# Optimization experiments

Measured on AMD Instinct MI355X. Metric: run time of the kernel, lower is better.

Reference implementation:

```python
import jax, jax.numpy as jnp
import numpy as np
from jax import lax

N_POINTS = 4_194_304
HIDDEN = 16
N_HIDDEN_LAYERS = 8   # num_layers=9 -> 1 input layer + 8 bias-free hidden layers


def setup_inputs() -> dict:
    key = jax.random.key(0)
    k_x, k_win, k_bin, k_wh, k_wout = jax.random.split(key, 5)
    x = jax.random.uniform(k_x, (N_POINTS, 2), dtype=jnp.float32)
    # PyTorch Linear default init: U(-1/sqrt(fan_in), 1/sqrt(fan_in))
    s_in = 1.0 / np.sqrt(2.0)
    s_h = 1.0 / np.sqrt(HIDDEN)
    W_in = jax.random.uniform(k_win, (HIDDEN, 2), jnp.float32, -s_in, s_in)
    b_in = jax.random.uniform(k_bin, (HIDDEN,), jnp.float32, -s_in, s_in)
    W_hidden = jax.random.uniform(k_wh, (N_HIDDEN_LAYERS, HIDDEN, HIDDEN), jnp.float32, -s_h, s_h)
    W_out = jax.random.uniform(k_wout, (3, HIDDEN), jnp.float32, -s_h, s_h)
    return {"x": x, "W_in": W_in, "b_in": b_in, "W_hidden": W_hidden, "W_out": W_out}


def reference(x, W_in, b_in, W_hidden, W_out):
    # [N,2] -> [N,16], biased input layer + tanh
    h = jnp.tanh(x @ W_in.T + b_in)
    # 8 bias-free 16x16 layers, each followed by tanh
    def step(h, W):
        return jnp.tanh(h @ W.T), None
    h, _ = lax.scan(step, h, W_hidden)
    # output layer 16 -> 3, sigmoid to map to [0,1] RGB
    return jax.nn.sigmoid(h @ W_out.T)
```

## Files before the change

kernel.cpp:

```cpp
#include <hip/hip_runtime.h>


typedef float  f32x4 __attribute__((ext_vector_type(4)));
typedef __fp16 f16x4 __attribute__((ext_vector_type(4)));
typedef __fp16 f16x2 __attribute__((ext_vector_type(2)));

#define K2   2.8853900817779268f
#define KOUT (-1.4426950408889634f)

__device__ __forceinline__ float tanh_from_y(float y) {
    float e = __builtin_amdgcn_exp2f(y);
    float r = __builtin_amdgcn_rcpf(e + 1.0f);
    return __builtin_fmaf(-2.0f, r, 1.0f);
}

__device__ __forceinline__ f16x4 pack4(float a, float b, float c, float d) {
    f16x2 lo = __builtin_amdgcn_cvt_pkrtz(a, b);
    f16x2 hi = __builtin_amdgcn_cvt_pkrtz(c, d);
    return __builtin_shufflevector(lo, hi, 0, 1, 2, 3);
}

__global__ __launch_bounds__(256, 4)
void artnet_kernel(const float2* __restrict__ x,
                   const float2* __restrict__ Win,
                   const float*  __restrict__ bin,
                   const float4* __restrict__ Wh,
                   const float4* __restrict__ Wout,
                   float* __restrict__ out,
                   int nPairs, int nWaves)
{
    const int tid  = blockIdx.x * 256 + threadIdx.x;
    const int gw   = tid >> 6;
    const int lane = threadIdx.x & 63;
    const int row  = lane & 15;
    const int quad = lane >> 4;

    f16x4 aw[8];
#pragma unroll
    for (int l = 0; l < 8; ++l) {
        float4 w = Wh[l * 64 + row * 4 + quad];
        aw[l] = pack4(w.x * K2, w.y * K2, w.z * K2, w.w * K2);
    }

    float wi0[4], wi1[4], bb[4];
#pragma unroll
    for (int j = 0; j < 4; ++j) {
        float2 wr = Win[quad * 4 + j];
        wi0[j] = wr.x * K2;
        wi1[j] = wr.y * K2;
        bb[j]  = bin[quad * 4 + j] * K2;
    }

    float wo0[4], wo1[4], wo2[4];
    {
        float4 w0 = Wout[0 * 4 + quad];
        float4 w1 = Wout[1 * 4 + quad];
        float4 w2 = Wout[2 * 4 + quad];
        wo0[0] = w0.x * KOUT; wo0[1] = w0.y * KOUT; wo0[2] = w0.z * KOUT; wo0[3] = w0.w * KOUT;
        wo1[0] = w1.x * KOUT; wo1[1] = w1.y * KOUT; wo1[2] = w1.z * KOUT; wo1[3] = w1.w * KOUT;
        wo2[0] = w2.x * KOUT; wo2[1] = w2.y * KOUT; wo2[2] = w2.z * KOUT; wo2[3] = w2.w * KOUT;
    }

    const f32x4 zero4 = {0.0f, 0.0f, 0.0f, 0.0f};

    for (int pi = gw; pi < nPairs; pi += nWaves) {
        const int t0 = pi * 2;
        f16x4 bf[2];
        float tl[2][4];

#pragma unroll
        for (int s = 0; s < 2; ++s) {
            float2 xv = x[(t0 + s) * 16 + row];
            float h0 = tanh_from_y(__builtin_fmaf(xv.x, wi0[0], __builtin_fmaf(xv.y, wi1[0], bb[0])));
            float h1 = tanh_from_y(__builtin_fmaf(xv.x, wi0[1], __builtin_fmaf(xv.y, wi1[1], bb[1])));
            float h2 = tanh_from_y(__builtin_fmaf(xv.x, wi0[2], __builtin_fmaf(xv.y, wi1[2], bb[2])));
            float h3 = tanh_from_y(__builtin_fmaf(xv.x, wi0[3], __builtin_fmaf(xv.y, wi1[3], bb[3])));
            bf[s] = pack4(h0, h1, h2, h3);
        }

#pragma unroll
        for (int l = 0; l < 8; ++l) {
#pragma unroll
            for (int s = 0; s < 2; ++s) {
                f32x4 acc = __builtin_amdgcn_mfma_f32_16x16x16f16(aw[l], bf[s], zero4, 0, 0, 0);
                float u0 = tanh_from_y(acc[0]);
                float u1 = tanh_from_y(acc[1]);
                float u2 = tanh_from_y(acc[2]);
                float u3 = tanh_from_y(acc[3]);
                bf[s] = pack4(u0, u1, u2, u3);
                if (l == 7) { tl[s][0] = u0; tl[s][1] = u1; tl[s][2] = u2; tl[s][3] = u3; }
            }
        }

#pragma unroll
        for (int s = 0; s < 2; ++s) {
            float p0 = 0.0f, p1 = 0.0f, p2 = 0.0f;
#pragma unroll
            for (int j = 0; j < 4; ++j) {
                p0 = __builtin_fmaf(tl[s][j], wo0[j], p0);
                p1 = __builtin_fmaf(tl[s][j], wo1[j], p1);
                p2 = __builtin_fmaf(tl[s][j], wo2[j], p2);
            }
            p0 += __shfl_xor(p0, 16, 64); p0 += __shfl_xor(p0, 32, 64);
            p1 += __shfl_xor(p1, 16, 64); p1 += __shfl_xor(p1, 32, 64);
            p2 += __shfl_xor(p2, 16, 64); p2 += __shfl_xor(p2, 32, 64);
            float y  = (quad == 0) ? p0 : ((quad == 1) ? p1 : p2);
            float e  = __builtin_amdgcn_exp2f(y);
            float sg = __builtin_amdgcn_rcpf(e + 1.0f);
            if (quad < 3) {
                out[((t0 + s) * 16 + row) * 3 + quad] = sg;
            }
        }
    }
}

extern "C" void kernel_launch(void* const* d_in, const int* in_sizes, int n_in,
                              void* d_out, int out_size, void* d_ws, size_t ws_size,
                              hipStream_t stream) {
    const float2* x    = (const float2*)d_in[0];
    const float2* Win  = (const float2*)d_in[1];
    const float*  bin  = (const float*) d_in[2];
    const float4* Wh   = (const float4*)d_in[3];
    const float4* Wout = (const float4*)d_in[4];
    float* out = (float*)d_out;

    const int n      = in_sizes[0] / 2;
    const int nPairs = n / 32;
    const int blocks = 1024;
    const int nWaves = blocks * 4;

    artnet_kernel<<<blocks, 256, 0, stream>>>(x, Win, bin, Wh, Wout, out, nPairs, nWaves);
}
```

Measured before the change: 218.4 us.

## Replace fp32 exp/rcp tanh with packed fp16 rational tanh approximation

Swaps the per-element fp32 exp2+rcp tanh for a packed-half Padé-style rational approximation that evaluates two lanes at once and shares one reciprocal between the two denominators. Weights are now prescaled by 0.25 instead of 2/ln2 to fit the rational's argument scaling. This cuts transcendental-unit pressure, which limits this MLP's throughput. It also raises the launch to 4096 blocks with 8 waves per SIMD bound. The cost is lower accuracy (fp16 arithmetic, no range clamp for large inputs) and possible fp16 overflow in the shared product q.x*q.y.

```diff
diff --git a/kernel.cpp b/kernel.cpp
--- a/kernel.cpp
+++ b/kernel.cpp
@@ -5,22 +5,42 @@
 typedef __fp16 f16x4 __attribute__((ext_vector_type(4)));
 typedef __fp16 f16x2 __attribute__((ext_vector_type(2)));
 
-#define K2   2.8853900817779268f
 #define KOUT (-1.4426950408889634f)
+#define QSC  0.25f
 
-__device__ __forceinline__ float tanh_from_y(float y) {
-    float e = __builtin_amdgcn_exp2f(y);
-    float r = __builtin_amdgcn_rcpf(e + 1.0f);
-    return __builtin_fmaf(-2.0f, r, 1.0f);
+__device__ __forceinline__ f16x2 splat2(float v) {
+    __fp16 h = (__fp16)v;
+    f16x2 r = {h, h};
+    return r;
 }
 
-__device__ __forceinline__ f16x4 pack4(float a, float b, float c, float d) {
-    f16x2 lo = __builtin_amdgcn_cvt_pkrtz(a, b);
-    f16x2 hi = __builtin_amdgcn_cvt_pkrtz(c, d);
-    return __builtin_shufflevector(lo, hi, 0, 1, 2, 3);
+__device__ __forceinline__ f16x2 pk_tanh(f16x2 zq) {
+    const f16x2 C0 = splat2(4.0f);
+    const f16x2 C1 = splat2(8.2051282f);
+    const f16x2 C2 = splat2(2.8643390f);
+    const f16x2 C3 = splat2(0.12124357f);
+    const f16x2 D1 = splat2(7.3846154f);
+    const f16x2 D2 = splat2(5.9673662f);
+    const f16x2 D3 = splat2(0.84869012f);
+    const f16x2 ONE = splat2(1.0f);
+
+    f16x2 u = zq * zq;
+    f16x2 p = C3 * u + C2;
+    p = p * u + C1;
+    p = p * u + C0;
+    f16x2 q = D3 * u + D2;
+    q = q * u + D1;
+    q = q * u + ONE;
+    f16x2 n = zq * p;
+    __fp16 qq = q.x * q.y;
+    __fp16 r  = __builtin_amdgcn_rcph(qq);
+    f16x2 qs  = __builtin_shufflevector(q, q, 1, 0);
+    f16x2 rr  = {r, r};
+    f16x2 inv = rr * qs;
+    return n * inv;
 }
 
-__global__ __launch_bounds__(256, 4)
+__global__ __launch_bounds__(256, 8)
 void artnet_kernel(const float2* __restrict__ x,
                    const float2* __restrict__ Win,
                    const float*  __restrict__ bin,
@@ -39,16 +59,18 @@
 #pragma unroll
     for (int l = 0; l < 8; ++l) {
         float4 w = Wh[l * 64 + row * 4 + quad];
-        aw[l] = pack4(w.x * K2, w.y * K2, w.z * K2, w.w * K2);
+        f16x2 lo = __builtin_amdgcn_cvt_pkrtz(w.x * QSC, w.y * QSC);
+        f16x2 hi = __builtin_amdgcn_cvt_pkrtz(w.z * QSC, w.w * QSC);
+        aw[l] = __builtin_shufflevector(lo, hi, 0, 1, 2, 3);
     }
 
     float wi0[4], wi1[4], bb[4];
 #pragma unroll
     for (int j = 0; j < 4; ++j) {
         float2 wr = Win[quad * 4 + j];
-        wi0[j] = wr.x * K2;
-        wi1[j] = wr.y * K2;
-        bb[j]  = bin[quad * 4 + j] * K2;
+        wi0[j] = wr.x * QSC;
+        wi1[j] = wr.y * QSC;
+        bb[j]  = bin[quad * 4 + j] * QSC;
     }
 
     float wo0[4], wo1[4], wo2[4];
@@ -66,16 +88,18 @@
     for (int pi = gw; pi < nPairs; pi += nWaves) {
         const int t0 = pi * 2;
         f16x4 bf[2];
-        float tl[2][4];
+        f16x2 last01[2], last23[2];
 
 #pragma unroll
         for (int s = 0; s < 2; ++s) {
             float2 xv = x[(t0 + s) * 16 + row];
-            float h0 = tanh_from_y(__builtin_fmaf(xv.x, wi0[0], __builtin_fmaf(xv.y, wi1[0], bb[0])));
-            float h1 = tanh_from_y(__builtin_fmaf(xv.x, wi0[1], __builtin_fmaf(xv.y, wi1[1], bb[1])));
-            float h2 = tanh_from_y(__builtin_fmaf(xv.x, wi0[2], __builtin_fmaf(xv.y, wi1[2], bb[2])));
-            float h3 = tanh_from_y(__builtin_fmaf(xv.x, wi0[3], __builtin_fmaf(xv.y, wi1[3], bb[3])));
-            bf[s] = pack4(h0, h1, h2, h3);
+            float h0 = __builtin_fmaf(xv.x, wi0[0], __builtin_fmaf(xv.y, wi1[0], bb[0]));
+            float h1 = __builtin_fmaf(xv.x, wi0[1], __builtin_fmaf(xv.y, wi1[1], bb[1]));
+            float h2 = __builtin_fmaf(xv.x, wi0[2], __builtin_fmaf(xv.y, wi1[2], bb[2]));
+            float h3 = __builtin_fmaf(xv.x, wi0[3], __builtin_fmaf(xv.y, wi1[3], bb[3]));
+            f16x2 t01 = pk_tanh(__builtin_amdgcn_cvt_pkrtz(h0, h1));
+            f16x2 t23 = pk_tanh(__builtin_amdgcn_cvt_pkrtz(h2, h3));
+            bf[s] = __builtin_shufflevector(t01, t23, 0, 1, 2, 3);
         }
 
 #pragma unroll
@@ -83,23 +107,24 @@
 #pragma unroll
             for (int s = 0; s < 2; ++s) {
                 f32x4 acc = __builtin_amdgcn_mfma_f32_16x16x16f16(aw[l], bf[s], zero4, 0, 0, 0);
-                float u0 = tanh_from_y(acc[0]);
-                float u1 = tanh_from_y(acc[1]);
-                float u2 = tanh_from_y(acc[2]);
-                float u3 = tanh_from_y(acc[3]);
-                bf[s] = pack4(u0, u1, u2, u3);
-                if (l == 7) { tl[s][0] = u0; tl[s][1] = u1; tl[s][2] = u2; tl[s][3] = u3; }
+                f16x2 t01 = pk_tanh(__builtin_amdgcn_cvt_pkrtz(acc[0], acc[1]));
+                f16x2 t23 = pk_tanh(__builtin_amdgcn_cvt_pkrtz(acc[2], acc[3]));
+                bf[s] = __builtin_shufflevector(t01, t23, 0, 1, 2, 3);
+                if (l == 7) { last01[s] = t01; last23[s] = t23; }
             }
         }
 
 #pragma unroll
         for (int s = 0; s < 2; ++s) {
+            float tl[4];
+            tl[0] = (float)last01[s].x; tl[1] = (float)last01[s].y;
+            tl[2] = (float)last23[s].x; tl[3] = (float)last23[s].y;
             float p0 = 0.0f, p1 = 0.0f, p2 = 0.0f;
 #pragma unroll
             for (int j = 0; j < 4; ++j) {
-                p0 = __builtin_fmaf(tl[s][j], wo0[j], p0);
-                p1 = __builtin_fmaf(tl[s][j], wo1[j], p1);
-                p2 = __builtin_fmaf(tl[s][j], wo2[j], p2);
+                p0 = __builtin_fmaf(tl[j], wo0[j], p0);
+                p1 = __builtin_fmaf(tl[j], wo1[j], p1);
+                p2 = __builtin_fmaf(tl[j], wo2[j], p2);
             }
             p0 += __shfl_xor(p0, 16, 64); p0 += __shfl_xor(p0, 32, 64);
             p1 += __shfl_xor(p1, 16, 64); p1 += __shfl_xor(p1, 32, 64);
@@ -126,7 +151,7 @@
 
     const int n      = in_sizes[0] / 2;
     const int nPairs = n / 32;
-    const int blocks = 1024;
+    const int blocks = 4096;
     const int nWaves = blocks * 4;
 
     artnet_kernel<<<blocks, 256, 0, stream>>>(x, Win, bin, Wh, Wout, out, nPairs, nWaves);
```

Measured after the change: 219.4 us. Within noise of the previous version (+0.4%).

## Replace exp/rcp tanh with packed rational approximation and MFMA output layer

Applied to the files above, without the earlier changes.

Swaps the transcendental tanh (exp2 plus reciprocal per element) for a packed-float2 rational polynomial that shares one reciprocal across four elements, with weights prescaled by 0.25 so the polynomial sees a scaled argument. The output layer becomes an MFMA with the output weights packed into rows 0-2, replacing the FMA-plus-shuffle reduction. Occupancy hints and grid size are also raised. The goal is to shift load off the slow transcendental unit and cut shuffle overhead, at the cost of a tanh approximation that is less exact (no clamping for large inputs) and an fp16-rounded output layer.

```diff
diff --git a/kernel.cpp b/kernel.cpp
--- a/kernel.cpp
+++ b/kernel.cpp
@@ -2,25 +2,56 @@
 
 
 typedef float  f32x4 __attribute__((ext_vector_type(4)));
+typedef float  f32x2 __attribute__((ext_vector_type(2)));
 typedef __fp16 f16x4 __attribute__((ext_vector_type(4)));
 typedef __fp16 f16x2 __attribute__((ext_vector_type(2)));
 
-#define K2   2.8853900817779268f
 #define KOUT (-1.4426950408889634f)
+#define QSC  0.25f
 
-__device__ __forceinline__ float tanh_from_y(float y) {
-    float e = __builtin_amdgcn_exp2f(y);
-    float r = __builtin_amdgcn_rcpf(e + 1.0f);
-    return __builtin_fmaf(-2.0f, r, 1.0f);
-}
+__device__ __forceinline__ f16x4 tanh4(f32x2 za, f32x2 zb) {
+    const f32x2 C0 = {4.0f, 4.0f};
+    const f32x2 C1 = {8.2051282f, 8.2051282f};
+    const f32x2 C2 = {2.8643390f, 2.8643390f};
+    const f32x2 C3 = {0.12124357f, 0.12124357f};
+    const f32x2 D1 = {7.3846154f, 7.3846154f};
+    const f32x2 D2 = {5.9673662f, 5.9673662f};
+    const f32x2 D3 = {0.84869012f, 0.84869012f};
+    const f32x2 ONE = {1.0f, 1.0f};
 
-__device__ __forceinline__ f16x4 pack4(float a, float b, float c, float d) {
-    f16x2 lo = __builtin_amdgcn_cvt_pkrtz(a, b);
-    f16x2 hi = __builtin_amdgcn_cvt_pkrtz(c, d);
+    f32x2 ua = za * za;
+    f32x2 ub = zb * zb;
+    f32x2 pa = __builtin_elementwise_fma(ua, C3, C2);
+    f32x2 pb = __builtin_elementwise_fma(ub, C3, C2);
+    pa = __builtin_elementwise_fma(ua, pa, C1);
+    pb = __builtin_elementwise_fma(ub, pb, C1);
+    pa = __builtin_elementwise_fma(ua, pa, C0);
+    pb = __builtin_elementwise_fma(ub, pb, C0);
+    f32x2 qa = __builtin_elementwise_fma(ua, D3, D2);
+    f32x2 qb = __builtin_elementwise_fma(ub, D3, D2);
+    qa = __builtin_elementwise_fma(ua, qa, D1);
+    qb = __builtin_elementwise_fma(ub, qb, D1);
+    qa = __builtin_elementwise_fma(ua, qa, ONE);
+    qb = __builtin_elementwise_fma(ub, qb, ONE);
+    f32x2 na = za * pa;
+    f32x2 nb = zb * pb;
+    float qqa = qa.x * qa.y;
+    float qqb = qb.x * qb.y;
+    float r   = __builtin_amdgcn_rcpf(qqa * qqb);
+    float ra  = r * qqb;
+    float rb  = r * qqa;
+    f32x2 rra = {ra, ra};
+    f32x2 rrb = {rb, rb};
+    f32x2 qas = {qa.y, qa.x};
+    f32x2 qbs = {qb.y, qb.x};
+    f32x2 ta = na * (rra * qas);
+    f32x2 tb = nb * (rrb * qbs);
+    f16x2 lo = __builtin_amdgcn_cvt_pkrtz(ta.x, ta.y);
+    f16x2 hi = __builtin_amdgcn_cvt_pkrtz(tb.x, tb.y);
     return __builtin_shufflevector(lo, hi, 0, 1, 2, 3);
 }
 
-__global__ __launch_bounds__(256, 4)
+__global__ __launch_bounds__(256, 8)
 void artnet_kernel(const float2* __restrict__ x,
                    const float2* __restrict__ Win,
                    const float*  __restrict__ bin,
@@ -39,26 +70,29 @@
 #pragma unroll
     for (int l = 0; l < 8; ++l) {
         float4 w = Wh[l * 64 + row * 4 + quad];
-        aw[l] = pack4(w.x * K2, w.y * K2, w.z * K2, w.w * K2);
+        f16x2 lo = __builtin_amdgcn_cvt_pkrtz(w.x * QSC, w.y * QSC);
+        f16x2 hi = __builtin_amdgcn_cvt_pkrtz(w.z * QSC, w.w * QSC);
+        aw[l] = __builtin_shufflevector(lo, hi, 0, 1, 2, 3);
     }
 
-    float wi0[4], wi1[4], bb[4];
-#pragma unroll
-    for (int j = 0; j < 4; ++j) {
-        float2 wr = Win[quad * 4 + j];
-        wi0[j] = wr.x * K2;
-        wi1[j] = wr.y * K2;
-        bb[j]  = bin[quad * 4 + j] * K2;
+    f16x4 awo = {(__fp16)0.0f, (__fp16)0.0f, (__fp16)0.0f, (__fp16)0.0f};
+    if (row < 3) {
+        float4 w = Wout[row * 4 + quad];
+        f16x2 lo = __builtin_amdgcn_cvt_pkrtz(w.x * KOUT, w.y * KOUT);
+        f16x2 hi = __builtin_amdgcn_cvt_pkrtz(w.z * KOUT, w.w * KOUT);
+        awo = __builtin_shufflevector(lo, hi, 0, 1, 2, 3);
     }
 
-    float wo0[4], wo1[4], wo2[4];
+    f32x2 w0a, w0b, w1a, w1b, bba, bbb;
     {
-        float4 w0 = Wout[0 * 4 + quad];
-        float4 w1 = Wout[1 * 4 + quad];
-        float4 w2 = Wout[2 * 4 + quad];
-        wo0[0] = w0.x * KOUT; wo0[1] = w0.y * KOUT; wo0[2] = w0.z * KOUT; wo0[3] = w0.w * KOUT;
-        wo1[0] = w1.x * KOUT; wo1[1] = w1.y * KOUT; wo1[2] = w1.z * KOUT; wo1[3] = w1.w * KOUT;
-        wo2[0] = w2.x * KOUT; wo2[1] = w2.y * KOUT; wo2[2] = w2.z * KOUT; wo2[3] = w2.w * KOUT;
+        float2 wr0 = Win[quad * 4 + 0], wr1 = Win[quad * 4 + 1];
+        float2 wr2 = Win[quad * 4 + 2], wr3 = Win[quad * 4 + 3];
+        w0a = (f32x2){wr0.x * QSC, wr1.x * QSC};
+        w0b = (f32x2){wr2.x * QSC, wr3.x * QSC};
+        w1a = (f32x2){wr0.y * QSC, wr1.y * QSC};
+        w1b = (f32x2){wr2.y * QSC, wr3.y * QSC};
+        bba = (f32x2){bin[quad * 4 + 0] * QSC, bin[quad * 4 + 1] * QSC};
+        bbb = (f32x2){bin[quad * 4 + 2] * QSC, bin[quad * 4 + 3] * QSC};
     }
 
     const f32x4 zero4 = {0.0f, 0.0f, 0.0f, 0.0f};
@@ -66,16 +100,15 @@
     for (int pi = gw; pi < nPairs; pi += nWaves) {
         const int t0 = pi * 2;
         f16x4 bf[2];
-        float tl[2][4];
 
 #pragma unroll
         for (int s = 0; s < 2; ++s) {
             float2 xv = x[(t0 + s) * 16 + row];
-            float h0 = tanh_from_y(__builtin_fmaf(xv.x, wi0[0], __builtin_fmaf(xv.y, wi1[0], bb[0])));
-            float h1 = tanh_from_y(__builtin_fmaf(xv.x, wi0[1], __builtin_fmaf(xv.y, wi1[1], bb[1])));
-            float h2 = tanh_from_y(__builtin_fmaf(xv.x, wi0[2], __builtin_fmaf(xv.y, wi1[2], bb[2])));
-            float h3 = tanh_from_y(__builtin_fmaf(xv.x, wi0[3], __builtin_fmaf(xv.y, wi1[3], bb[3])));
-            bf[s] = pack4(h0, h1, h2, h3);
+            f32x2 xx = {xv.x, xv.x};
+            f32x2 yy = {xv.y, xv.y};
+            f32x2 h01 = __builtin_elementwise_fma(xx, w0a, __builtin_elementwise_fma(yy, w1a, bba));
+            f32x2 h23 = __builtin_elementwise_fma(xx, w0b, __builtin_elementwise_fma(yy, w1b, bbb));
+            bf[s] = tanh4(h01, h23);
         }
 
 #pragma unroll
@@ -83,32 +116,20 @@
 #pragma unroll
             for (int s = 0; s < 2; ++s) {
                 f32x4 acc = __builtin_amdgcn_mfma_f32_16x16x16f16(aw[l], bf[s], zero4, 0, 0, 0);
-                float u0 = tanh_from_y(acc[0]);
-                float u1 = tanh_from_y(acc[1]);
-                float u2 = tanh_from_y(acc[2]);
-                float u3 = tanh_from_y(acc[3]);
-                bf[s] = pack4(u0, u1, u2, u3);
-                if (l == 7) { tl[s][0] = u0; tl[s][1] = u1; tl[s][2] = u2; tl[s][3] = u3; }
+                bf[s] = tanh4((f32x2){acc[0], acc[1]}, (f32x2){acc[2], acc[3]});
             }
         }
 
 #pragma unroll
         for (int s = 0; s < 2; ++s) {
-            float p0 = 0.0f, p1 = 0.0f, p2 = 0.0f;
+            f32x4 acco = __builtin_amdgcn_mfma_f32_16x16x16f16(awo, bf[s], zero4, 0, 0, 0);
+            if (quad == 0) {
+                const int p = (t0 + s) * 16 + row;
 #pragma unroll
-            for (int j = 0; j < 4; ++j) {
-                p0 = __builtin_fmaf(tl[s][j], wo0[j], p0);
-                p1 = __builtin_fmaf(tl[s][j], wo1[j], p1);
-                p2 = __builtin_fmaf(tl[s][j], wo2[j], p2);
-            }
-            p0 += __shfl_xor(p0, 16, 64); p0 += __shfl_xor(p0, 32, 64);
-            p1 += __shfl_xor(p1, 16, 64); p1 += __shfl_xor(p1, 32, 64);
-            p2 += __shfl_xor(p2, 16, 64); p2 += __shfl_xor(p2, 32, 64);
-            float y  = (quad == 0) ? p0 : ((quad == 1) ? p1 : p2);
-            float e  = __builtin_amdgcn_exp2f(y);
-            float sg = __builtin_amdgcn_rcpf(e + 1.0f);
-            if (quad < 3) {
-                out[((t0 + s) * 16 + row) * 3 + quad] = sg;
+                for (int i = 0; i < 3; ++i) {
+                    float e = __builtin_amdgcn_exp2f(acco[i]);
+                    out[p * 3 + i] = __builtin_amdgcn_rcpf(e + 1.0f);
+                }
             }
         }
     }
@@ -126,7 +147,7 @@
 
     const int n      = in_sizes[0] / 2;
     const int nPairs = n / 32;
-    const int blocks = 1024;
+    const int blocks = 4096;
     const int nWaves = blocks * 4;
 
     artnet_kernel<<<blocks, 256, 0, stream>>>(x, Win, bin, Wh, Wout, out, nPairs, nWaves);
```

Result: slower. 247.0 us (+13.1%).
